# Optimization experiments

Measured on AMD Instinct MI355X. Metric: run time of the kernel, lower is better.

## Reference

```python
import jax, jax.numpy as jnp
import numpy as np

L, E, H, C, N = 3, 512, 8, 64, 65536
DH = E // H
LN_EPS = 1e-5


def setup_inputs() -> dict:
    key = jax.random.key(0)
    ks = jax.random.split(key, 10)
    s = 1.0 / np.sqrt(E)
    return {
        "support_features": jax.random.normal(ks[0], (N, E), jnp.float32),
        "support_labels": jax.random.randint(ks[1], (N,), 0, C),
        "W1": jax.random.normal(ks[2], (L, E, E), jnp.float32) * s,
        "b1": jnp.zeros((L, E), jnp.float32),
        "gamma": jnp.ones((L, E), jnp.float32),
        "beta": jnp.zeros((L, E), jnp.float32),
        "W2": jax.random.normal(ks[3], (L, E, E), jnp.float32) * s,
        "b2": jnp.zeros((L, E), jnp.float32),
        "Wq": jax.random.normal(ks[4], (E, E), jnp.float32) * s,
        "bq": jnp.zeros((E,), jnp.float32),
        "Wk": jax.random.normal(ks[5], (E, E), jnp.float32) * s,
        "bk": jnp.zeros((E,), jnp.float32),
        "Wv": jax.random.normal(ks[6], (E, E), jnp.float32) * s,
        "bv": jnp.zeros((E,), jnp.float32),
        "Wo": jax.random.normal(ks[7], (E, E), jnp.float32) * s,
        "bo": jnp.zeros((E,), jnp.float32),
        "level_weights": jnp.ones((L,), jnp.float32) / L,
        "level_temps": jnp.ones((L,), jnp.float32),
    }


def _layer_norm(x, g, b):
    mu = jnp.mean(x, axis=-1, keepdims=True)
    var = jnp.var(x, axis=-1, keepdims=True)
    return (x - mu) * jax.lax.rsqrt(var + LN_EPS) * g + b


def reference(support_features, support_labels, W1, b1, gamma, beta, W2, b2,
              Wq, bq, Wk, bk, Wv, bv, Wo, bo, level_weights, level_temps):
    # class membership mask [C, N]; segment counts [C]
    onehot = support_labels[None, :] == jnp.arange(C)[:, None]
    counts = jnp.sum(onehot, axis=1).astype(support_features.dtype)
    scale = 1.0 / np.sqrt(DH)
    protos = []
    for l in range(L):  # small fixed number of levels
        # prototype MLP (dropout inactive at eval)
        h = jnp.maximum(_layer_norm(support_features @ W1[l] + b1[l], gamma[l], beta[l]), 0.0)
        feat = h @ W2[l] + b2[l]                              # [N, E]
        # per-class mean context (segment mean) -> query
        ctx = (onehot.astype(feat.dtype) @ feat) / counts[:, None]  # [C, E]
        q = (ctx @ Wq + bq).reshape(C, H, DH)
        k = (feat @ Wk + bk).reshape(N, H, DH)
        v = (feat @ Wv + bv).reshape(N, H, DH)
        scores = jnp.einsum('chd,nhd->chn', q, k) * scale      # [C, H, N]
        scores = jnp.where(onehot[:, None, :], scores, -jnp.inf)
        attn = jax.nn.softmax(scores, axis=-1)
        out = jnp.einsum('chn,nhd->chd', attn, v).reshape(C, E)
        protos.append(out @ Wo + bo)                           # [C, E]
    lw = jax.nn.softmax(level_weights)
    final = protos[0] * (lw[0] / level_temps[0])
    for i in range(1, L):
        final = final + protos[i] * (lw[i] / level_temps[i])
    return final
```

## Files before the change

### kernel.cpp

```cpp
#include <hip/hip_runtime.h>
#include <math.h>

#define N_SUP 65536
#define E_DIM 512
#define H_HEADS 8
#define C_CLS 64
#define DHD 64
#define L_LEV 3
#define LN_EPS 1e-5f
#define ATTN_SPLITS 4
#define SCAT_BLOCKS 256
#define KV_LD 1024

typedef _Float16 f16x8 __attribute__((ext_vector_type(8)));
typedef _Float16 f16x4 __attribute__((ext_vector_type(4)));
typedef float f32x4 __attribute__((ext_vector_type(4)));

__device__ __forceinline__ void gload_lds16(const void* g, void* lds) {
    __builtin_amdgcn_global_load_lds((const __attribute__((address_space(1))) void*)g,
                                     (__attribute__((address_space(3))) void*)lds,
                                     16, 0, 0);
}

__global__ __launch_bounds__(256)
void hgemm_bt(const _Float16* __restrict__ A, int lda, size_t aStride,
              const _Float16* __restrict__ Bt, size_t btStride,
              const float* __restrict__ bias, size_t biasStride,
              _Float16* __restrict__ C, int ldc, size_t cStride, int nCol) {
    const int z = blockIdx.y;
    A += z * aStride; Bt += z * btStride; bias += z * biasStride; C += z * cStride;

    const int nRow = gridDim.x / nCol;
    const int R = nRow < 64 ? nRow : 64;
    const int bid = blockIdx.x;
    const int bandSz = R * nCol;
    const int band = bid / bandSz;
    const int rem = bid % bandSz;
    const int colT = rem / R;
    const int rowT = band * R + (rem % R);

    __shared__ _Float16 As[128][32];
    __shared__ _Float16 Bs[128][32];
    const int tid = threadIdx.x;
    const int wave = tid >> 6, lane = tid & 63;
    const int row0 = rowT * 128, col0 = colT * 128;
    const int wm = (wave & 1) * 64, wn = (wave >> 1) * 64;

    const int ci0 = wave * 128 + lane, ci1 = ci0 + 64;
    const int r0 = ci0 >> 2, gc0 = (ci0 & 3) ^ ((r0 >> 1) & 3);
    const int r1 = ci1 >> 2, gc1 = (ci1 & 3) ^ ((r1 >> 1) & 3);
    const _Float16* Ar0 = A + (size_t)(row0 + r0) * lda + gc0 * 8;
    const _Float16* Ar1 = A + (size_t)(row0 + r1) * lda + gc1 * 8;
    const _Float16* Br0 = Bt + (size_t)(col0 + r0) * E_DIM + gc0 * 8;
    const _Float16* Br1 = Bt + (size_t)(col0 + r1) * E_DIM + gc1 * 8;
    char* ldsA = (char*)&As[0][0] + wave * 2048;
    char* ldsB = (char*)&Bs[0][0] + wave * 2048;

    const int m = lane & 15, q = lane >> 4;
    const int koff = ((q ^ ((m >> 1) & 3))) * 8;

    f32x4 acc[4][4];
#pragma unroll
    for (int i = 0; i < 4; ++i)
#pragma unroll
        for (int j = 0; j < 4; ++j) acc[i][j] = (f32x4){0.f, 0.f, 0.f, 0.f};

    for (int k0 = 0; k0 < E_DIM; k0 += 32) {
        gload_lds16(Ar0 + k0, ldsA);
        gload_lds16(Ar1 + k0, ldsA + 1024);
        gload_lds16(Br0 + k0, ldsB);
        gload_lds16(Br1 + k0, ldsB + 1024);
        __syncthreads();

        f16x8 af[4], bf[4];
#pragma unroll
        for (int i = 0; i < 4; ++i)
            af[i] = *(const f16x8*)&As[wm + i * 16 + m][koff];
#pragma unroll
        for (int j = 0; j < 4; ++j)
            bf[j] = *(const f16x8*)&Bs[wn + j * 16 + m][koff];
#pragma unroll
        for (int i = 0; i < 4; ++i)
#pragma unroll
            for (int j = 0; j < 4; ++j)
                acc[i][j] = __builtin_amdgcn_mfma_f32_16x16x32_f16(af[i], bf[j], acc[i][j], 0, 0, 0);
        __syncthreads();
    }

#pragma unroll
    for (int i = 0; i < 4; ++i) {
        const int rbase = row0 + wm + i * 16 + q * 4;
#pragma unroll
        for (int j = 0; j < 4; ++j) {
            const int col = col0 + wn + j * 16 + m;
            const float bv = bias[col];
#pragma unroll
            for (int r = 0; r < 4; ++r)
                C[(size_t)(rbase + r) * ldc + col] = (_Float16)(acc[i][j][r] + bv);
        }
    }
}

__global__ __launch_bounds__(256)
void conv32to16(const float* __restrict__ in, _Float16* __restrict__ out, int n4) {
    int i = blockIdx.x * 256 + threadIdx.x;
    if (i < n4) {
        f32x4 v = ((const f32x4*)in)[i];
        f16x4 o = {(_Float16)v[0], (_Float16)v[1], (_Float16)v[2], (_Float16)v[3]};
        ((f16x4*)out)[i] = o;
    }
}

__global__ __launch_bounds__(256)
void transpose_all(const float* __restrict__ W1, const float* __restrict__ Wk,
                   const float* __restrict__ Wv, const float* __restrict__ Wq,
                   _Float16* __restrict__ W1allT, _Float16* __restrict__ WkvqT) {
    const int z = blockIdx.z;
    const float* src;
    _Float16* dst;
    const size_t MSZ = (size_t)E_DIM * E_DIM;
    if (z < 3)       { src = W1 + z * MSZ; dst = W1allT + z * MSZ; }
    else if (z == 3) { src = Wk;           dst = WkvqT; }
    else if (z == 4) { src = Wv;           dst = WkvqT + MSZ; }
    else             { src = Wq;           dst = WkvqT + 2 * MSZ; }

    __shared__ float t[32][33];
    const int k0 = blockIdx.x * 32, n0 = blockIdx.y * 32;
    const int tx = threadIdx.x & 31, ty = threadIdx.x >> 5;
#pragma unroll
    for (int r = 0; r < 32; r += 8)
        t[ty + r][tx] = src[(size_t)(k0 + ty + r) * E_DIM + n0 + tx];
    __syncthreads();
#pragma unroll
    for (int r = 0; r < 32; r += 8)
        dst[(size_t)(n0 + ty + r) * E_DIM + k0 + tx] = (_Float16)t[tx][ty + r];
}

__global__ __launch_bounds__(256)
void bias_compose(const float* __restrict__ b2, const float* __restrict__ Wk,
                  const float* __restrict__ Wv, const float* __restrict__ Wq,
                  const float* __restrict__ bk, const float* __restrict__ bv,
                  const float* __restrict__ bq, float* __restrict__ bcomp) {
    const int l = blockIdx.y;
    const int n = blockIdx.x * 256 + threadIdx.x;
    const float* W; const float* bb; int nn;
    if (n < 512)       { W = Wk; bb = bk; nn = n; }
    else if (n < 1024) { W = Wv; bb = bv; nn = n - 512; }
    else               { W = Wq; bb = bq; nn = n - 1024; }
    float acc = 0.f;
    for (int j = 0; j < E_DIM; ++j)
        acc = fmaf(b2[l * E_DIM + j], W[(size_t)j * E_DIM + nn], acc);
    bcomp[l * 1536 + n] = acc + bb[nn];
}

__global__ __launch_bounds__(256)
void ln_relu_all(_Float16* __restrict__ P, const float* __restrict__ gamma,
                 const float* __restrict__ beta) {
    const int row = blockIdx.x * 4 + (threadIdx.x >> 6);
    const int l = blockIdx.y;
    const int lane = threadIdx.x & 63;
    _Float16* prow = P + (size_t)row * (L_LEV * E_DIM) + l * E_DIM + lane * 8;
    const float* g = gamma + l * E_DIM + lane * 8;
    const float* b = beta  + l * E_DIM + lane * 8;
    f16x8 v = *(const f16x8*)prow;
    float x[8];
    float s = 0.f, s2 = 0.f;
#pragma unroll
    for (int e = 0; e < 8; ++e) {
        x[e] = (float)v[e];
        s += x[e];
        s2 = fmaf(x[e], x[e], s2);
    }
#pragma unroll
    for (int off = 32; off; off >>= 1) {
        s  += __shfl_xor(s, off);
        s2 += __shfl_xor(s2, off);
    }
    const float mean = s * (1.f / E_DIM);
    const float var  = s2 * (1.f / E_DIM) - mean * mean;
    const float rstd = rsqrtf(var + LN_EPS);
    f32x4 g0 = *(const f32x4*)g;
    f32x4 g1 = *(const f32x4*)(g + 4);
    f32x4 b0 = *(const f32x4*)b;
    f32x4 b1 = *(const f32x4*)(b + 4);
    f16x8 o;
#pragma unroll
    for (int e = 0; e < 4; ++e) {
        o[e]     = (_Float16)fmaxf(fmaf((x[e]     - mean) * rstd, g0[e], b0[e]), 0.f);
        o[e + 4] = (_Float16)fmaxf(fmaf((x[e + 4] - mean) * rstd, g1[e], b1[e]), 0.f);
    }
    *(f16x8*)prow = o;
}

__global__ __launch_bounds__(256)
void label_block_hist(const int* __restrict__ labels, int* __restrict__ blockCounts) {
    __shared__ int h[C_CLS];
    const int tid = threadIdx.x;
    if (tid < C_CLS) h[tid] = 0;
    __syncthreads();
    atomicAdd(&h[labels[blockIdx.x * 256 + tid]], 1);
    __syncthreads();
    if (tid < C_CLS) blockCounts[blockIdx.x * C_CLS + tid] = h[tid];
}

__global__ __launch_bounds__(64)
void scan_offsets(const int* __restrict__ blockCounts, int* __restrict__ counts,
                  int* __restrict__ offs, int* __restrict__ blockOffs) {
    const int c = threadIdx.x;
    int total = 0;
    for (int b = 0; b < SCAT_BLOCKS; ++b) total += blockCounts[b * C_CLS + c];
    counts[c] = total;
    __shared__ int tot[C_CLS];
    tot[c] = total;
    __syncthreads();
    int off = 0;
    for (int cc = 0; cc < c; ++cc) off += tot[cc];
    offs[c] = off;
    if (c == C_CLS - 1) offs[C_CLS] = off + total;
    int run = off;
    for (int b = 0; b < SCAT_BLOCKS; ++b) {
        blockOffs[b * C_CLS + c] = run;
        run += blockCounts[b * C_CLS + c];
    }
}

__global__ __launch_bounds__(256)
void scatter_sorted(const int* __restrict__ labels, const int* __restrict__ blockOffs,
                    int* __restrict__ members) {
    __shared__ int cur[C_CLS];
    const int tid = threadIdx.x;
    if (tid < C_CLS) cur[tid] = blockOffs[blockIdx.x * C_CLS + tid];
    __syncthreads();
    const int i = blockIdx.x * 256 + tid;
    const int c = labels[i];
    const int p = atomicAdd(&cur[c], 1);
    members[p] = i;
}

__global__ __launch_bounds__(256)
void zero_f32(float* __restrict__ p, int n) {
    int i = blockIdx.x * 256 + threadIdx.x;
    if (i < n) p[i] = 0.f;
}

#define CTX_SPLITS 8
__global__ __launch_bounds__(256)
void ctx_sum_kernel(const _Float16* __restrict__ src, int ld,
                    const int* __restrict__ members, const int* __restrict__ offsets,
                    float* __restrict__ hsum) {
    const int c = blockIdx.x, split = blockIdx.y;
    const int tid = threadIdx.x;
    const int wave = tid >> 6, lane = tid & 63;
    const int start = offsets[c], end = offsets[c + 1];
    const int wg = split * 4 + wave;
    const int stride = 4 * CTX_SPLITS;

    float acc[8];
#pragma unroll
    for (int e = 0; e < 8; ++e) acc[e] = 0.f;

    int i = start + wg;
    for (; i + stride < end; i += 2 * stride) {
        const int n0 = members[i];
        const int n1 = members[i + stride];
        f16x8 r0 = *(const f16x8*)(src + (size_t)n0 * ld + lane * 8);
        f16x8 r1 = *(const f16x8*)(src + (size_t)n1 * ld + lane * 8);
#pragma unroll
        for (int e = 0; e < 8; ++e) acc[e] += (float)r0[e] + (float)r1[e];
    }
    if (i < end) {
        const int n0 = members[i];
        f16x8 r0 = *(const f16x8*)(src + (size_t)n0 * ld + lane * 8);
#pragma unroll
        for (int e = 0; e < 8; ++e) acc[e] += (float)r0[e];
    }

    __shared__ float red[4][64][8];
#pragma unroll
    for (int e = 0; e < 8; ++e) red[wave][lane][e] = acc[e];
    __syncthreads();
#pragma unroll
    for (int t = 0; t < 2; ++t) {
        const int col = tid * 2 + t;
        const int ln = col >> 3, e = col & 7;
        float s = red[0][ln][e] + red[1][ln][e] + red[2][ln][e] + red[3][ln][e];
        atomicAdd(&hsum[c * E_DIM + col], s);
    }
}

__global__ __launch_bounds__(256)
void row_gemm_q(const float* __restrict__ hsum, const int* __restrict__ counts,
                const _Float16* __restrict__ W2qT, const float* __restrict__ bias,
                float* __restrict__ q) {
    const int c = blockIdx.x;
    const int tid = threadIdx.x;
    const float inv = 1.f / (float)counts[c];
    __shared__ float xrow[E_DIM];
    xrow[tid]       = hsum[c * E_DIM + tid] * inv;
    xrow[tid + 256] = hsum[c * E_DIM + tid + 256] * inv;
    __syncthreads();
    const int n0 = tid, n1 = tid + 256;
    float a0 = 0.f, a1 = 0.f;
#pragma unroll 4
    for (int k0 = 0; k0 < E_DIM; k0 += 8) {
        f16x8 w0 = *(const f16x8*)(W2qT + (size_t)n0 * E_DIM + k0);
        f16x8 w1 = *(const f16x8*)(W2qT + (size_t)n1 * E_DIM + k0);
#pragma unroll
        for (int e = 0; e < 8; ++e) {
            const float xv = xrow[k0 + e];
            a0 = fmaf(xv, (float)w0[e], a0);
            a1 = fmaf(xv, (float)w1[e], a1);
        }
    }
    q[c * E_DIM + n0] = a0 + bias[n0];
    q[c * E_DIM + n1] = a1 + bias[n1];
}

__global__ __launch_bounds__(256)
void attn_partial(const float* __restrict__ q, const _Float16* __restrict__ kv,
                  const int* __restrict__ members, const int* __restrict__ offsets,
                  float* __restrict__ pm, float* __restrict__ pl,
                  float* __restrict__ po) {
    const int c = blockIdx.x, h = blockIdx.y, s = blockIdx.z;
    const int tid = threadIdx.x;
    const int wave = tid >> 6, lane = tid & 63;
    const int start = offsets[c], end = offsets[c + 1];
    const int g = s * 4 + wave;

    const float* qrow = q + c * E_DIM + h * DHD;
    float qv[64];
#pragma unroll
    for (int d = 0; d < 64; ++d) qv[d] = qrow[d];

    __shared__ float ps[4][64];
    float m = -INFINITY, lsum = 0.f, out = 0.f;

    for (int ch0 = start + g * 64; ch0 < end; ch0 += 16 * 64) {
        const int nvalid = min(64, end - ch0);
        const int idx = ch0 + lane;
        const int mi = members[idx < end ? idx : end - 1];
        const _Float16* krow = kv + (size_t)mi * KV_LD + h * DHD;
        float dot = 0.f;
#pragma unroll
        for (int j = 0; j < 8; ++j) {
            f16x8 kr = *(const f16x8*)(krow + j * 8);
#pragma unroll
            for (int e = 0; e < 8; ++e)
                dot = fmaf((float)kr[e], qv[j * 8 + e], dot);
        }
        float sc = (lane < nvalid) ? dot * 0.125f : -INFINITY;
        float cm = sc;
#pragma unroll
        for (int off = 32; off; off >>= 1) cm = fmaxf(cm, __shfl_xor(cm, off));
        const float nm = fmaxf(m, cm);
        const float alpha = __expf(m - nm);
        const float p = (lane < nvalid) ? __expf(sc - nm) : 0.f;
        ps[wave][lane] = p;
        out *= alpha;
        lsum *= alpha;
        m = nm;
        asm volatile("" ::: "memory");
#pragma unroll 16
        for (int j = 0; j < 64; ++j) {
            const int nj = __shfl(mi, j);
            const float pj = ps[wave][j];
            const float vv = (float)kv[(size_t)nj * KV_LD + E_DIM + h * DHD + lane];
            out = fmaf(pj, vv, out);
            lsum += pj;
        }
    }

    __shared__ float rm[4], rl[4], racc[4][64];
    racc[wave][lane] = out;
    if (lane == 0) { rm[wave] = m; rl[wave] = lsum; }
    __syncthreads();
    if (wave == 0) {
        float M = fmaxf(fmaxf(rm[0], rm[1]), fmaxf(rm[2], rm[3]));
        float o = 0.f, Lt = 0.f;
#pragma unroll
        for (int w = 0; w < 4; ++w) {
            float al = __expf(rm[w] - M);
            o  += al * racc[w][lane];
            Lt += al * rl[w];
        }
        const int pidx = (c * H_HEADS + h) * ATTN_SPLITS + s;
        po[pidx * 64 + lane] = o;
        if (lane == 0) { pm[pidx] = M; pl[pidx] = Lt; }
    }
}

__global__ __launch_bounds__(64)
void attn_combine(const float* __restrict__ pm, const float* __restrict__ pl,
                  const float* __restrict__ po, float* __restrict__ attn_out) {
    const int ch = blockIdx.x;
    const int lane = threadIdx.x;
    float M = -INFINITY;
#pragma unroll
    for (int s = 0; s < ATTN_SPLITS; ++s) M = fmaxf(M, pm[ch * ATTN_SPLITS + s]);
    float o = 0.f, Lt = 0.f;
#pragma unroll
    for (int s = 0; s < ATTN_SPLITS; ++s) {
        const int pidx = ch * ATTN_SPLITS + s;
        float al = __expf(pm[pidx] - M);
        o  += al * po[pidx * 64 + lane];
        Lt += al * pl[pidx];
    }
    attn_out[ch * DHD + lane] = o / Lt;
}

__global__ __launch_bounds__(256)
void proto_accum(const float* __restrict__ attn_out, const float* __restrict__ Wo,
                 const float* __restrict__ bo, const float* __restrict__ lvlw,
                 const float* __restrict__ lvlt, int l, float* __restrict__ out) {
    const int c = blockIdx.x;
    const int tid = threadIdx.x;
    __shared__ float xrow[E_DIM];
    xrow[tid]       = attn_out[c * E_DIM + tid];
    xrow[tid + 256] = attn_out[c * E_DIM + tid + 256];
    __syncthreads();
    float a0 = 0.f, a1 = 0.f;
#pragma unroll 8
    for (int k = 0; k < E_DIM; ++k) {
        float cv = xrow[k];
        a0 = fmaf(cv, Wo[(size_t)k * E_DIM + tid], a0);
        a1 = fmaf(cv, Wo[(size_t)k * E_DIM + tid + 256], a1);
    }
    float w0 = lvlw[0], w1 = lvlw[1], w2 = lvlw[2];
    float mx = fmaxf(w0, fmaxf(w1, w2));
    float e0 = expf(w0 - mx), e1 = expf(w1 - mx), e2 = expf(w2 - mx);
    float ssum = e0 + e1 + e2;
    float lw = (l == 0 ? e0 : (l == 1 ? e1 : e2)) / ssum;
    float coef = lw / lvlt[l];
    float r0 = (a0 + bo[tid]) * coef;
    float r1 = (a1 + bo[tid + 256]) * coef;
    if (l == 0) {
        out[c * E_DIM + tid]       = r0;
        out[c * E_DIM + tid + 256] = r1;
    } else {
        out[c * E_DIM + tid]       += r0;
        out[c * E_DIM + tid + 256] += r1;
    }
}

extern "C" void kernel_launch(void* const* d_in, const int* in_sizes, int n_in,
                              void* d_out, int out_size, void* d_ws, size_t ws_size,
                              hipStream_t stream) {
    const float* X      = (const float*)d_in[0];
    const int*   labels = (const int*)  d_in[1];
    const float* W1     = (const float*)d_in[2];
    const float* b1     = (const float*)d_in[3];
    const float* gamma  = (const float*)d_in[4];
    const float* beta   = (const float*)d_in[5];
    const float* W2     = (const float*)d_in[6];
    const float* b2     = (const float*)d_in[7];
    const float* Wq     = (const float*)d_in[8];
    const float* bq     = (const float*)d_in[9];
    const float* Wk     = (const float*)d_in[10];
    const float* bk     = (const float*)d_in[11];
    const float* Wv     = (const float*)d_in[12];
    const float* bv     = (const float*)d_in[13];
    const float* Wo     = (const float*)d_in[14];
    const float* bo     = (const float*)d_in[15];
    const float* lvlw   = (const float*)d_in[16];
    const float* lvlt   = (const float*)d_in[17];
    float* out = (float*)d_out;

    char* p = (char*)d_ws;
    const size_t MSZ = (size_t)E_DIM * E_DIM;
    _Float16* Xh      = (_Float16*)p; p += (size_t)N_SUP * E_DIM * 2;
    _Float16* bufPall = (_Float16*)p; p += (size_t)N_SUP * E_DIM * L_LEV * 2;
    _Float16* bufKV   = (_Float16*)p; p += (size_t)N_SUP * KV_LD * 2;
    _Float16* W1allT  = (_Float16*)p; p += L_LEV * MSZ * 2;
    _Float16* WkvqT   = (_Float16*)p; p += 3 * MSZ * 2;
    _Float16* W2f16   = (_Float16*)p; p += L_LEV * MSZ * 2;
    _Float16* W2compT = (_Float16*)p; p += (size_t)L_LEV * 1536 * E_DIM * 2;
    float* zeros512 = (float*)p; p += E_DIM * sizeof(float);
    float* bcomp = (float*)p; p += L_LEV * 1536 * sizeof(float);
    float* hsum  = (float*)p; p += C_CLS * E_DIM * sizeof(float);
    float* qb    = (float*)p; p += C_CLS * E_DIM * sizeof(float);
    float* ao    = (float*)p; p += C_CLS * E_DIM * sizeof(float);
    float* pm    = (float*)p; p += C_CLS * H_HEADS * ATTN_SPLITS * sizeof(float);
    float* pl    = (float*)p; p += C_CLS * H_HEADS * ATTN_SPLITS * sizeof(float);
    float* po    = (float*)p; p += C_CLS * H_HEADS * ATTN_SPLITS * 64 * sizeof(float);
    int* counts      = (int*)p; p += 256;
    int* offs        = (int*)p; p += 512;
    int* members     = (int*)p; p += (size_t)N_SUP * sizeof(int);
    int* blockCounts = (int*)p; p += (size_t)SCAT_BLOCKS * C_CLS * sizeof(int);
    int* blockOffs   = (int*)p; p += (size_t)SCAT_BLOCKS * C_CLS * sizeof(int);

    label_block_hist<<<SCAT_BLOCKS, 256, 0, stream>>>(labels, blockCounts);
    scan_offsets<<<1, 64, 0, stream>>>(blockCounts, counts, offs, blockOffs);
    scatter_sorted<<<SCAT_BLOCKS, 256, 0, stream>>>(labels, blockOffs, members);

    conv32to16<<<(N_SUP * E_DIM / 4) / 256, 256, 0, stream>>>(X, Xh, N_SUP * E_DIM / 4);
    conv32to16<<<(int)(L_LEV * MSZ / 4 / 256), 256, 0, stream>>>(W2, W2f16, L_LEV * MSZ / 4);
    transpose_all<<<dim3(16, 16, 6), 256, 0, stream>>>(W1, Wk, Wv, Wq, W1allT, WkvqT);
    zero_f32<<<2, 256, 0, stream>>>(zeros512, E_DIM);

    hgemm_bt<<<dim3(12 * 4, L_LEV), 256, 0, stream>>>(
        WkvqT, E_DIM, 0, W2f16, MSZ, zeros512, 0,
        W2compT, E_DIM, (size_t)1536 * E_DIM, 4);
    bias_compose<<<dim3(6, L_LEV), 256, 0, stream>>>(b2, Wk, Wv, Wq, bk, bv, bq, bcomp);

    const int nRow = N_SUP / 128;
    hgemm_bt<<<dim3(nRow * 12, 1), 256, 0, stream>>>(
        Xh, E_DIM, 0, W1allT, 0, b1, 0, bufPall, L_LEV * E_DIM, 0, 12);
    ln_relu_all<<<dim3(N_SUP / 4, L_LEV), 256, 0, stream>>>(bufPall, gamma, beta);

    for (int l = 0; l < L_LEV; ++l) {
        hgemm_bt<<<dim3(nRow * 8, 1), 256, 0, stream>>>(
            bufPall + (size_t)l * E_DIM, L_LEV * E_DIM, 0,
            W2compT + (size_t)l * 1536 * E_DIM, 0,
            bcomp + l * 1536, 0, bufKV, KV_LD, 0, 8);
        zero_f32<<<(C_CLS * E_DIM) / 256, 256, 0, stream>>>(hsum, C_CLS * E_DIM);
        ctx_sum_kernel<<<dim3(C_CLS, CTX_SPLITS), 256, 0, stream>>>(
            bufPall + (size_t)l * E_DIM, L_LEV * E_DIM, members, offs, hsum);
        row_gemm_q<<<C_CLS, 256, 0, stream>>>(
            hsum, counts, W2compT + (size_t)l * 1536 * E_DIM + (size_t)1024 * E_DIM,
            bcomp + l * 1536 + 1024, qb);
        attn_partial<<<dim3(C_CLS, H_HEADS, ATTN_SPLITS), 256, 0, stream>>>(
            qb, bufKV, members, offs, pm, pl, po);
        attn_combine<<<C_CLS * H_HEADS, 64, 0, stream>>>(pm, pl, po, ao);
        proto_accum<<<C_CLS, 256, 0, stream>>>(ao, Wo, bo, lvlw, lvlt, l, out);
    }
}
```

Measured before the change: 1.086 ms.

## Batch context sums across levels, fuse attn combine into proto, widen attention splits

Context sums and the q projection for all three levels now run in single launches before the level loop. Per-split partial sums are written to a buffer instead of being atomically added, which removes the zero kernel and the atomics. The attention-combine kernel is folded into proto_accum, and attention uses 8 splits instead of 4, with guards so that waves with no work skip their q load and are ignored in the merge. The result is fewer launches and more parallelism in exchange for larger partial buffers and an extra reduction pass.

```diff
diff --git a/kernel.cpp b/kernel.cpp
--- a/kernel.cpp
+++ b/kernel.cpp
@@ -8,7 +8,8 @@
 #define DHD 64
 #define L_LEV 3
 #define LN_EPS 1e-5f
-#define ATTN_SPLITS 4
+#define ATTN_SPLITS 8
+#define CTX_SPLITS 16
 #define SCAT_BLOCKS 256
 #define KV_LD 1024
 
@@ -243,17 +244,17 @@
     if (i < n) p[i] = 0.f;
 }
 
-#define CTX_SPLITS 8
-__global__ __launch_bounds__(256)
-void ctx_sum_kernel(const _Float16* __restrict__ src, int ld,
-                    const int* __restrict__ members, const int* __restrict__ offsets,
-                    float* __restrict__ hsum) {
-    const int c = blockIdx.x, split = blockIdx.y;
+__global__ __launch_bounds__(256)
+void ctx_partial(const _Float16* __restrict__ P, const int* __restrict__ members,
+                 const int* __restrict__ offsets, float* __restrict__ hpart) {
+    const int c = blockIdx.x, split = blockIdx.y, l = blockIdx.z;
+    const _Float16* src = P + (size_t)l * E_DIM;
     const int tid = threadIdx.x;
     const int wave = tid >> 6, lane = tid & 63;
     const int start = offsets[c], end = offsets[c + 1];
     const int wg = split * 4 + wave;
     const int stride = 4 * CTX_SPLITS;
+    const int ld = L_LEV * E_DIM;
 
     float acc[8];
 #pragma unroll
@@ -279,32 +280,42 @@
 #pragma unroll
     for (int e = 0; e < 8; ++e) red[wave][lane][e] = acc[e];
     __syncthreads();
+    float* dst = hpart + (((size_t)l * C_CLS + c) * CTX_SPLITS + split) * E_DIM;
 #pragma unroll
     for (int t = 0; t < 2; ++t) {
         const int col = tid * 2 + t;
         const int ln = col >> 3, e = col & 7;
-        float s = red[0][ln][e] + red[1][ln][e] + red[2][ln][e] + red[3][ln][e];
-        atomicAdd(&hsum[c * E_DIM + col], s);
-    }
-}
-
-__global__ __launch_bounds__(256)
-void row_gemm_q(const float* __restrict__ hsum, const int* __restrict__ counts,
-                const _Float16* __restrict__ W2qT, const float* __restrict__ bias,
+        dst[col] = red[0][ln][e] + red[1][ln][e] + red[2][ln][e] + red[3][ln][e];
+    }
+}
+
+__global__ __launch_bounds__(256)
+void row_gemm_q(const float* __restrict__ hpart, const int* __restrict__ counts,
+                const _Float16* __restrict__ W2compT, const float* __restrict__ bcomp,
                 float* __restrict__ q) {
-    const int c = blockIdx.x;
+    const int c = blockIdx.x, l = blockIdx.y;
     const int tid = threadIdx.x;
     const float inv = 1.f / (float)counts[c];
     __shared__ float xrow[E_DIM];
-    xrow[tid]       = hsum[c * E_DIM + tid] * inv;
-    xrow[tid + 256] = hsum[c * E_DIM + tid + 256] * inv;
-    __syncthreads();
+    const float* hp = hpart + ((size_t)l * C_CLS + c) * CTX_SPLITS * E_DIM;
+    float s0 = 0.f, s1 = 0.f;
+#pragma unroll
+    for (int s = 0; s < CTX_SPLITS; ++s) {
+        s0 += hp[s * E_DIM + tid];
+        s1 += hp[s * E_DIM + tid + 256];
+    }
+    xrow[tid]       = s0 * inv;
+    xrow[tid + 256] = s1 * inv;
+    __syncthreads();
+
+    const _Float16* Wq = W2compT + (size_t)l * 1536 * E_DIM + (size_t)1024 * E_DIM;
+    const float* bias = bcomp + l * 1536 + 1024;
     const int n0 = tid, n1 = tid + 256;
     float a0 = 0.f, a1 = 0.f;
 #pragma unroll 4
     for (int k0 = 0; k0 < E_DIM; k0 += 8) {
-        f16x8 w0 = *(const f16x8*)(W2qT + (size_t)n0 * E_DIM + k0);
-        f16x8 w1 = *(const f16x8*)(W2qT + (size_t)n1 * E_DIM + k0);
+        f16x8 w0 = *(const f16x8*)(Wq + (size_t)n0 * E_DIM + k0);
+        f16x8 w1 = *(const f16x8*)(Wq + (size_t)n1 * E_DIM + k0);
 #pragma unroll
         for (int e = 0; e < 8; ++e) {
             const float xv = xrow[k0 + e];
@@ -312,8 +323,9 @@
             a1 = fmaf(xv, (float)w1[e], a1);
         }
     }
-    q[c * E_DIM + n0] = a0 + bias[n0];
-    q[c * E_DIM + n1] = a1 + bias[n1];
+    float* qq = q + (size_t)l * C_CLS * E_DIM;
+    qq[c * E_DIM + n0] = a0 + bias[n0];
+    qq[c * E_DIM + n1] = a1 + bias[n1];
 }
 
 __global__ __launch_bounds__(256)
@@ -327,15 +339,18 @@
     const int start = offsets[c], end = offsets[c + 1];
     const int g = s * 4 + wave;
 
-    const float* qrow = q + c * E_DIM + h * DHD;
     float qv[64];
-#pragma unroll
-    for (int d = 0; d < 64; ++d) qv[d] = qrow[d];
+    const bool active = (start + g * 64) < end;
+    if (active) {
+        const float* qrow = q + c * E_DIM + h * DHD;
+#pragma unroll
+        for (int d = 0; d < 64; ++d) qv[d] = qrow[d];
+    }
 
     __shared__ float ps[4][64];
     float m = -INFINITY, lsum = 0.f, out = 0.f;
 
-    for (int ch0 = start + g * 64; ch0 < end; ch0 += 16 * 64) {
+    for (int ch0 = start + g * 64; ch0 < end; ch0 += 4 * ATTN_SPLITS * 64) {
         const int nvalid = min(64, end - ch0);
         const int idx = ch0 + lane;
         const int mi = members[idx < end ? idx : end - 1];
@@ -379,7 +394,7 @@
         float o = 0.f, Lt = 0.f;
 #pragma unroll
         for (int w = 0; w < 4; ++w) {
-            float al = __expf(rm[w] - M);
+            const float al = (rm[w] > -INFINITY) ? __expf(rm[w] - M) : 0.f;
             o  += al * racc[w][lane];
             Lt += al * rl[w];
         }
@@ -389,35 +404,33 @@
     }
 }
 
-__global__ __launch_bounds__(64)
-void attn_combine(const float* __restrict__ pm, const float* __restrict__ pl,
-                  const float* __restrict__ po, float* __restrict__ attn_out) {
-    const int ch = blockIdx.x;
-    const int lane = threadIdx.x;
-    float M = -INFINITY;
-#pragma unroll
-    for (int s = 0; s < ATTN_SPLITS; ++s) M = fmaxf(M, pm[ch * ATTN_SPLITS + s]);
-    float o = 0.f, Lt = 0.f;
-#pragma unroll
-    for (int s = 0; s < ATTN_SPLITS; ++s) {
-        const int pidx = ch * ATTN_SPLITS + s;
-        float al = __expf(pm[pidx] - M);
-        o  += al * po[pidx * 64 + lane];
-        Lt += al * pl[pidx];
-    }
-    attn_out[ch * DHD + lane] = o / Lt;
-}
-
-__global__ __launch_bounds__(256)
-void proto_accum(const float* __restrict__ attn_out, const float* __restrict__ Wo,
+__global__ __launch_bounds__(256)
+void proto_accum(const float* __restrict__ pm, const float* __restrict__ pl,
+                 const float* __restrict__ po, const float* __restrict__ Wo,
                  const float* __restrict__ bo, const float* __restrict__ lvlw,
                  const float* __restrict__ lvlt, int l, float* __restrict__ out) {
     const int c = blockIdx.x;
     const int tid = threadIdx.x;
+    const int wave = tid >> 6, lane = tid & 63;
     __shared__ float xrow[E_DIM];
-    xrow[tid]       = attn_out[c * E_DIM + tid];
-    xrow[tid + 256] = attn_out[c * E_DIM + tid + 256];
-    __syncthreads();
+#pragma unroll
+    for (int hh = wave; hh < H_HEADS; hh += 4) {
+        const int ch = c * H_HEADS + hh;
+        float M = -INFINITY;
+#pragma unroll
+        for (int s = 0; s < ATTN_SPLITS; ++s) M = fmaxf(M, pm[ch * ATTN_SPLITS + s]);
+        float o = 0.f, Lt = 0.f;
+#pragma unroll
+        for (int s = 0; s < ATTN_SPLITS; ++s) {
+            const int pidx = ch * ATTN_SPLITS + s;
+            const float al = (pm[pidx] > -INFINITY) ? __expf(pm[pidx] - M) : 0.f;
+            o  += al * po[pidx * 64 + lane];
+            Lt += al * pl[pidx];
+        }
+        xrow[hh * 64 + lane] = o / Lt;
+    }
+    __syncthreads();
+
     float a0 = 0.f, a1 = 0.f;
 #pragma unroll 8
     for (int k = 0; k < E_DIM; ++k) {
@@ -476,12 +489,11 @@
     _Float16* W2compT = (_Float16*)p; p += (size_t)L_LEV * 1536 * E_DIM * 2;
     float* zeros512 = (float*)p; p += E_DIM * sizeof(float);
     float* bcomp = (float*)p; p += L_LEV * 1536 * sizeof(float);
-    float* hsum  = (float*)p; p += C_CLS * E_DIM * sizeof(float);
-    float* qb    = (float*)p; p += C_CLS * E_DIM * sizeof(float);
-    float* ao    = (float*)p; p += C_CLS * E_DIM * sizeof(float);
+    float* hpart = (float*)p; p += (size_t)L_LEV * C_CLS * CTX_SPLITS * E_DIM * sizeof(float);
+    float* qb    = (float*)p; p += (size_t)L_LEV * C_CLS * E_DIM * sizeof(float);
     float* pm    = (float*)p; p += C_CLS * H_HEADS * ATTN_SPLITS * sizeof(float);
     float* pl    = (float*)p; p += C_CLS * H_HEADS * ATTN_SPLITS * sizeof(float);
-    float* po    = (float*)p; p += C_CLS * H_HEADS * ATTN_SPLITS * 64 * sizeof(float);
+    float* po    = (float*)p; p += (size_t)C_CLS * H_HEADS * ATTN_SPLITS * 64 * sizeof(float);
     int* counts      = (int*)p; p += 256;
     int* offs        = (int*)p; p += 512;
     int* members     = (int*)p; p += (size_t)N_SUP * sizeof(int);
@@ -507,20 +519,18 @@
         Xh, E_DIM, 0, W1allT, 0, b1, 0, bufPall, L_LEV * E_DIM, 0, 12);
     ln_relu_all<<<dim3(N_SUP / 4, L_LEV), 256, 0, stream>>>(bufPall, gamma, beta);
 
+    ctx_partial<<<dim3(C_CLS, CTX_SPLITS, L_LEV), 256, 0, stream>>>(
+        bufPall, members, offs, hpart);
+    row_gemm_q<<<dim3(C_CLS, L_LEV), 256, 0, stream>>>(
+        hpart, counts, W2compT, bcomp, qb);
+
     for (int l = 0; l < L_LEV; ++l) {
         hgemm_bt<<<dim3(nRow * 8, 1), 256, 0, stream>>>(
             bufPall + (size_t)l * E_DIM, L_LEV * E_DIM, 0,
             W2compT + (size_t)l * 1536 * E_DIM, 0,
             bcomp + l * 1536, 0, bufKV, KV_LD, 0, 8);
-        zero_f32<<<(C_CLS * E_DIM) / 256, 256, 0, stream>>>(hsum, C_CLS * E_DIM);
-        ctx_sum_kernel<<<dim3(C_CLS, CTX_SPLITS), 256, 0, stream>>>(
-            bufPall + (size_t)l * E_DIM, L_LEV * E_DIM, members, offs, hsum);
-        row_gemm_q<<<C_CLS, 256, 0, stream>>>(
-            hsum, counts, W2compT + (size_t)l * 1536 * E_DIM + (size_t)1024 * E_DIM,
-            bcomp + l * 1536 + 1024, qb);
         attn_partial<<<dim3(C_CLS, H_HEADS, ATTN_SPLITS), 256, 0, stream>>>(
-            qb, bufKV, members, offs, pm, pl, po);
-        attn_combine<<<C_CLS * H_HEADS, 64, 0, stream>>>(pm, pl, po, ao);
-        proto_accum<<<C_CLS, 256, 0, stream>>>(ao, Wo, bo, lvlw, lvlt, l, out);
-    }
-}
+            qb + (size_t)l * C_CLS * E_DIM, bufKV, members, offs, pm, pl, po);
+        proto_accum<<<C_CLS, 256, 0, stream>>>(pm, pl, po, Wo, bo, lvlw, lvlt, l, out);
+    }
+}
```

New measurement: 1.003 ms. 1.08x faster.
